# Kernel tuning notes

Measured on AMD Instinct MI355X. Metric: run time of the kernel, lower is better.

The kernel has to match this reference:

```python
import jax, jax.numpy as jnp
import numpy as np

IN_DIM = 1024
HID = 2048
BATCH = 8192


def setup_inputs() -> dict:
    key = jax.random.key(0)
    ks = jax.random.split(key, 10)
    s1 = 1.0 / np.sqrt(IN_DIM)
    s2 = 1.0 / np.sqrt(HID)
    inp = {
        "x": jax.random.normal(ks[0], (BATCH, IN_DIM), dtype=jnp.float32),
        "W1": jax.random.uniform(ks[1], (IN_DIM, HID), jnp.float32, -s1, s1),
        "b1": jax.random.uniform(ks[2], (HID,), jnp.float32, -s1, s1),
        "W2": jax.random.uniform(ks[3], (HID, HID), jnp.float32, -s2, s2),
        "b2": jax.random.uniform(ks[4], (HID,), jnp.float32, -s2, s2),
        "W3": jax.random.uniform(ks[5], (HID, HID), jnp.float32, -s2, s2),
        "b3": jax.random.uniform(ks[6], (HID,), jnp.float32, -s2, s2),
        "Wout": jax.random.uniform(ks[7], (HID, 1), jnp.float32, -s2, s2),
        "bout": jax.random.uniform(ks[8], (1,), jnp.float32, -s2, s2),
        "weight": jnp.array([0.1], dtype=jnp.float32),
        "bias": jnp.array([0.0], dtype=jnp.float32),
        "scale": jnp.array([1.0], dtype=jnp.float32),
        "shift": jnp.array([0.0], dtype=jnp.float32),
    }
    return inp


def reference(x, W1, b1, W2, b2, W3, b3, Wout, bout, weight, bias, scale, shift):
    # 3-layer tanh MLP core
    h = jnp.tanh(x @ W1 + b1)
    h = jnp.tanh(h @ W2 + b2)
    core_out = jnp.tanh(h @ W3 + b3)  # [B, HID]
    # Closed form of per-element 1-qubit statevector sim:
    # <Y> for RX(w) RY(v) H |0>  ==  sin(w) * sin(v)
    q_out = jnp.sin(weight[0]) * jnp.sin(core_out)
    q_out = (q_out + bias[0]) * scale[0] + shift[0]
    out = core_out + q_out
    out = out @ Wout + bout  # [B, 1]
    return out.squeeze(-1)  # [B]
```

## Files before the change

kernel.cpp:

```cpp
#include <hip/hip_runtime.h>
#include <hip/hip_bf16.h>


typedef _Float16 f16;
typedef __attribute__((ext_vector_type(8))) _Float16 f16x8;
typedef __attribute__((ext_vector_type(4))) _Float16 f16x4;
typedef __attribute__((ext_vector_type(4))) float f32x4;

#define BATCH 8192
#define IN_DIM 1024
#define HID 2048

__device__ __forceinline__ float fast_tanh(float x) {
  x = fminf(12.0f, fmaxf(-12.0f, x));
  float e = __expf(2.0f * x);
  return (e - 1.0f) * __builtin_amdgcn_rcpf(e + 1.0f);
}

__global__ __launch_bounds__(256) void cast_kernel(const float* __restrict__ in,
                                                   f16* __restrict__ out, int n4) {
  int i = blockIdx.x * blockDim.x + threadIdx.x;
  if (i < n4) {
    float4 v = reinterpret_cast<const float4*>(in)[i];
    f16x4 o = { (f16)v.x, (f16)v.y, (f16)v.z, (f16)v.w };
    reinterpret_cast<f16x4*>(out)[i] = o;
  }
}

__global__ __launch_bounds__(256) void transpose_cast_kernel(const float* __restrict__ W,
                                                             f16* __restrict__ Wt,
                                                             int K, int N) {
  __shared__ float tile[32][33];
  int kb = blockIdx.y * 32, nb = blockIdx.x * 32;
  int tx = threadIdx.x, ty = threadIdx.y;
#pragma unroll
  for (int i = 0; i < 4; ++i)
    tile[ty + i * 8][tx] = W[(size_t)(kb + ty + i * 8) * N + nb + tx];
  __syncthreads();
#pragma unroll
  for (int i = 0; i < 4; ++i)
    Wt[(size_t)(nb + ty + i * 8) * K + kb + tx] = (f16)tile[tx][ty + i * 8];
}


#define GLDS16(g, l)                                                         \
  __builtin_amdgcn_global_load_lds(                                          \
      (const __attribute__((address_space(1))) unsigned int*)(g),            \
      (__attribute__((address_space(3))) unsigned int*)(l), 16, 0, 0)

template <int K>
__global__ __launch_bounds__(512, 2) void gemm256_bias_tanh(
    const f16* __restrict__ A,
    const f16* __restrict__ Bt,
    const float* __restrict__ bias,
    f16* __restrict__ Out) {
  constexpr int NT = K / 32;
  __shared__ f16 As[4][8192];
  __shared__ f16 Bs[4][8192];

  const int T = threadIdx.x;
  const int l = T & 63;
  const int w = T >> 6;
  const int wm = w >> 2, wn = w & 3;
  const int lr = l & 15;
  const int lc = l >> 4;

  const int bm = (int)blockIdx.x >> 3;
  const int bn = (int)blockIdx.x & 7;
  const int tm = bm << 8, tn = bn << 8;

  const int srow = ((T >> 5) << 3) + (T & 7);
  const int skel = ((T >> 3) & 3) << 3;
  const f16* gA0 = A + (size_t)(tm + srow) * K + skel;
  const f16* gA1 = A + (size_t)(tm + srow + 128) * K + skel;
  const f16* gB0 = Bt + (size_t)(tn + srow) * K + skel;
  const f16* gB1 = Bt + (size_t)(tn + srow + 128) * K + skel;
  const int ldsw0 = w * 512;
  const int ldsw1 = 4096 + w * 512;

  const int abase = (wm * 16 + (lr >> 3)) * 256 + lc * 64 + (lr & 7) * 8;
  const int bbase = (wn * 8 + (lr >> 3)) * 256 + lc * 64 + (lr & 7) * 8;

  f32x4 acc[8][4] = {};

  GLDS16(gA0, &As[0][ldsw0]);
  GLDS16(gA1, &As[0][ldsw1]);
  GLDS16(gB0, &Bs[0][ldsw0]);
  GLDS16(gB1, &Bs[0][ldsw1]);
  GLDS16(gA0 + 32, &As[1][ldsw0]);
  GLDS16(gA1 + 32, &As[1][ldsw1]);
  GLDS16(gB0 + 32, &Bs[1][ldsw0]);
  GLDS16(gB1 + 32, &Bs[1][ldsw1]);
  asm volatile("s_waitcnt vmcnt(4)" ::: "memory");
  __builtin_amdgcn_s_barrier();
  __builtin_amdgcn_sched_barrier(0);

  for (int t = 0; t < NT; ++t) {
    const int q = t & 3;
    f16x8 afr[4], bfr[4];
#pragma unroll
    for (int mi = 0; mi < 4; ++mi)
      afr[mi] = *reinterpret_cast<const f16x8*>(&As[q][abase + mi * 512]);
#pragma unroll
    for (int ni = 0; ni < 4; ++ni)
      bfr[ni] = *reinterpret_cast<const f16x8*>(&Bs[q][bbase + ni * 512]);
    if (t + 2 < NT) {
      const int q2 = (t + 2) & 3;
      const int ko = (t + 2) * 32;
      GLDS16(gA0 + ko, &As[q2][ldsw0]);
      GLDS16(gA1 + ko, &As[q2][ldsw1]);
    }
    __builtin_amdgcn_s_barrier();
    asm volatile("s_waitcnt lgkmcnt(0)" ::: "memory");
    __builtin_amdgcn_sched_barrier(0);
    __builtin_amdgcn_s_setprio(1);
#pragma unroll
    for (int mi = 0; mi < 4; ++mi)
#pragma unroll
      for (int ni = 0; ni < 4; ++ni)
        acc[mi][ni] = __builtin_amdgcn_mfma_f32_16x16x32_f16(
            afr[mi], bfr[ni], acc[mi][ni], 0, 0, 0);
    __builtin_amdgcn_s_setprio(0);
    __builtin_amdgcn_s_barrier();
    __builtin_amdgcn_sched_barrier(0);

    f16x8 afr2[4];
#pragma unroll
    for (int mi = 0; mi < 4; ++mi)
      afr2[mi] = *reinterpret_cast<const f16x8*>(&As[q][abase + (4 + mi) * 512]);
    if (t + 2 < NT) {
      const int q2 = (t + 2) & 3;
      const int ko = (t + 2) * 32;
      GLDS16(gB0 + ko, &Bs[q2][ldsw0]);
      GLDS16(gB1 + ko, &Bs[q2][ldsw1]);
      asm volatile("s_waitcnt vmcnt(4)" ::: "memory");
    } else {
      asm volatile("s_waitcnt vmcnt(0)" ::: "memory");
    }
    __builtin_amdgcn_s_barrier();
    asm volatile("s_waitcnt lgkmcnt(0)" ::: "memory");
    __builtin_amdgcn_sched_barrier(0);
    __builtin_amdgcn_s_setprio(1);
#pragma unroll
    for (int mi = 0; mi < 4; ++mi)
#pragma unroll
      for (int ni = 0; ni < 4; ++ni)
        acc[4 + mi][ni] = __builtin_amdgcn_mfma_f32_16x16x32_f16(
            afr2[mi], bfr[ni], acc[4 + mi][ni], 0, 0, 0);
    __builtin_amdgcn_s_setprio(0);
    __builtin_amdgcn_s_barrier();
    __builtin_amdgcn_sched_barrier(0);
  }

#pragma unroll
  for (int ni = 0; ni < 4; ++ni) {
    const int col = tn + wn * 64 + ni * 16 + lr;
    const float bv = bias[col];
#pragma unroll
    for (int mi = 0; mi < 8; ++mi) {
      const int row0 = tm + wm * 128 + mi * 16 + ((l >> 4) << 2);
#pragma unroll
      for (int j = 0; j < 4; ++j) {
        float v = fast_tanh(acc[mi][ni][j] + bv);
        Out[(size_t)(row0 + j) * HID + col] = (f16)v;
      }
    }
  }
}

__global__ __launch_bounds__(256) void final_reduce(
    const f16* __restrict__ core, const float* __restrict__ Wout,
    const float* __restrict__ bout, const float* __restrict__ weight,
    const float* __restrict__ qbias, const float* __restrict__ qscale,
    const float* __restrict__ qshift, float* __restrict__ out) {
  const int b = blockIdx.x, t = threadIdx.x;
  const float sw = __sinf(weight[0]);
  const float qb = qbias[0], qs = qscale[0], qsh = qshift[0];
  f16x8 c8 = *reinterpret_cast<const f16x8*>(&core[(size_t)b * HID + t * 8]);
  float sum = 0.f;
#pragma unroll
  for (int j = 0; j < 8; ++j) {
    float c = (float)c8[j];
    float s = c + (sw * __sinf(c) + qb) * qs + qsh;
    sum += s * Wout[t * 8 + j];
  }
#pragma unroll
  for (int off = 32; off >= 1; off >>= 1) sum += __shfl_down(sum, off, 64);
  __shared__ float red[4];
  if ((t & 63) == 0) red[t >> 6] = sum;
  __syncthreads();
  if (t == 0) out[b] = red[0] + red[1] + red[2] + red[3] + bout[0];
}

extern "C" void kernel_launch(void* const* d_in, const int* in_sizes, int n_in,
                              void* d_out, int out_size, void* d_ws, size_t ws_size,
                              hipStream_t stream) {
  const float* x    = (const float*)d_in[0];
  const float* W1   = (const float*)d_in[1];
  const float* b1   = (const float*)d_in[2];
  const float* W2   = (const float*)d_in[3];
  const float* b2   = (const float*)d_in[4];
  const float* W3   = (const float*)d_in[5];
  const float* b3   = (const float*)d_in[6];
  const float* Wout = (const float*)d_in[7];
  const float* bout = (const float*)d_in[8];
  const float* wgt  = (const float*)d_in[9];
  const float* qb   = (const float*)d_in[10];
  const float* qs   = (const float*)d_in[11];
  const float* qsh  = (const float*)d_in[12];
  float* out = (float*)d_out;

  char* ws = (char*)d_ws;
  size_t off = 0;
  f16* xh  = (f16*)(ws + off); off += (size_t)BATCH * IN_DIM * sizeof(f16);
  f16* w1t = (f16*)(ws + off); off += (size_t)HID * IN_DIM * sizeof(f16);
  f16* w2t = (f16*)(ws + off); off += (size_t)HID * HID * sizeof(f16);
  f16* w3t = (f16*)(ws + off); off += (size_t)HID * HID * sizeof(f16);
  f16* h1  = (f16*)(ws + off); off += (size_t)BATCH * HID * sizeof(f16);
  f16* h2  = (f16*)(ws + off); off += (size_t)BATCH * HID * sizeof(f16);

  {
    int n4 = BATCH * IN_DIM / 4;
    cast_kernel<<<(n4 + 255) / 256, 256, 0, stream>>>(x, xh, n4);
  }
  {
    dim3 blk(32, 8);
    transpose_cast_kernel<<<dim3(HID / 32, IN_DIM / 32), blk, 0, stream>>>(W1, w1t, IN_DIM, HID);
    transpose_cast_kernel<<<dim3(HID / 32, HID / 32),    blk, 0, stream>>>(W2, w2t, HID, HID);
    transpose_cast_kernel<<<dim3(HID / 32, HID / 32),    blk, 0, stream>>>(W3, w3t, HID, HID);
  }
  const int grid = (BATCH / 256) * (HID / 256);
  gemm256_bias_tanh<IN_DIM><<<grid, 512, 0, stream>>>(xh, w1t, b1, h1);
  gemm256_bias_tanh<HID>   <<<grid, 512, 0, stream>>>(h1, w2t, b2, h2);
  gemm256_bias_tanh<HID>   <<<grid, 512, 0, stream>>>(h2, w3t, b3, h1);
  final_reduce<<<BATCH, 256, 0, stream>>>(h1, Wout, bout, wgt, qb, qs, qsh, out);
}
```

Measured before the change: 362.2 us.

## Deepen GEMM prefetch to three stages, merge weight transposes, stage epilogue through LDS

The GEMM main loop now prefetches three K-tiles ahead and loads both A and B tiles in one step. It replaces the two half-step phases with a single 8x4 MFMA block per iteration and one barrier, cutting synchronisation overhead. The epilogue writes tanh outputs into swizzled LDS and then stores 16-byte coalesced rows instead of scattered 2-byte stores. The three weight transpose launches are merged into one kernel. Holding all 8 A fragments at once raises register pressure, which may hurt occupancy at 2 blocks per CU.

```diff
diff --git a/kernel.cpp b/kernel.cpp
--- a/kernel.cpp
+++ b/kernel.cpp
@@ -27,12 +27,19 @@
   }
 }
 
-__global__ __launch_bounds__(256) void transpose_cast_kernel(const float* __restrict__ W,
-                                                             f16* __restrict__ Wt,
-                                                             int K, int N) {
+__global__ __launch_bounds__(256) void transpose_cast3(
+    const float* __restrict__ W1, const float* __restrict__ W2,
+    const float* __restrict__ W3, f16* __restrict__ w1t,
+    f16* __restrict__ w2t, f16* __restrict__ w3t) {
   __shared__ float tile[32][33];
-  int kb = blockIdx.y * 32, nb = blockIdx.x * 32;
-  int tx = threadIdx.x, ty = threadIdx.y;
+  int b = blockIdx.x;
+  const float* W; f16* Wt; int K, N;
+  if (b < 2048)      { W = W1; Wt = w1t; K = IN_DIM; N = HID; }
+  else if (b < 6144) { W = W2; Wt = w2t; K = HID;    N = HID; b -= 2048; }
+  else               { W = W3; Wt = w3t; K = HID;    N = HID; b -= 6144; }
+  const int nbt = N / 32;
+  const int nb = (b % nbt) * 32, kb = (b / nbt) * 32;
+  const int tx = threadIdx.x, ty = threadIdx.y;
 #pragma unroll
   for (int i = 0; i < 4; ++i)
     tile[ty + i * 8][tx] = W[(size_t)(kb + ty + i * 8) * N + nb + tx];
@@ -55,8 +62,9 @@
     const float* __restrict__ bias,
     f16* __restrict__ Out) {
   constexpr int NT = K / 32;
-  __shared__ f16 As[4][8192];
-  __shared__ f16 Bs[4][8192];
+  __shared__ f16 smem[65536];
+  f16* As = smem;
+  f16* Bs = smem + 32768;
 
   const int T = threadIdx.x;
   const int l = T & 63;
@@ -83,88 +91,86 @@
 
   f32x4 acc[8][4] = {};
 
-  GLDS16(gA0, &As[0][ldsw0]);
-  GLDS16(gA1, &As[0][ldsw1]);
-  GLDS16(gB0, &Bs[0][ldsw0]);
-  GLDS16(gB1, &Bs[0][ldsw1]);
-  GLDS16(gA0 + 32, &As[1][ldsw0]);
-  GLDS16(gA1 + 32, &As[1][ldsw1]);
-  GLDS16(gB0 + 32, &Bs[1][ldsw0]);
-  GLDS16(gB1 + 32, &Bs[1][ldsw1]);
-  asm volatile("s_waitcnt vmcnt(4)" ::: "memory");
+#pragma unroll
+  for (int p = 0; p < 3; ++p) {
+    const int ko = p * 32;
+    f16* aq = As + p * 8192;
+    f16* bq = Bs + p * 8192;
+    GLDS16(gA0 + ko, aq + ldsw0);
+    GLDS16(gA1 + ko, aq + ldsw1);
+    GLDS16(gB0 + ko, bq + ldsw0);
+    GLDS16(gB1 + ko, bq + ldsw1);
+  }
+  asm volatile("s_waitcnt vmcnt(8)" ::: "memory");
   __builtin_amdgcn_s_barrier();
   __builtin_amdgcn_sched_barrier(0);
 
   for (int t = 0; t < NT; ++t) {
     const int q = t & 3;
-    f16x8 afr[4], bfr[4];
-#pragma unroll
-    for (int mi = 0; mi < 4; ++mi)
-      afr[mi] = *reinterpret_cast<const f16x8*>(&As[q][abase + mi * 512]);
+    const f16* aq = As + q * 8192;
+    const f16* bq = Bs + q * 8192;
+    f16x8 afr[8], bfr[4];
+#pragma unroll
+    for (int mi = 0; mi < 8; ++mi)
+      afr[mi] = *reinterpret_cast<const f16x8*>(&aq[abase + mi * 512]);
 #pragma unroll
     for (int ni = 0; ni < 4; ++ni)
-      bfr[ni] = *reinterpret_cast<const f16x8*>(&Bs[q][bbase + ni * 512]);
-    if (t + 2 < NT) {
-      const int q2 = (t + 2) & 3;
-      const int ko = (t + 2) * 32;
-      GLDS16(gA0 + ko, &As[q2][ldsw0]);
-      GLDS16(gA1 + ko, &As[q2][ldsw1]);
+      bfr[ni] = *reinterpret_cast<const f16x8*>(&bq[bbase + ni * 512]);
+    if (t + 3 < NT) {
+      const int q3 = (t + 3) & 3;
+      const int ko = (t + 3) * 32;
+      f16* aw = As + q3 * 8192;
+      f16* bw = Bs + q3 * 8192;
+      GLDS16(gA0 + ko, aw + ldsw0);
+      GLDS16(gA1 + ko, aw + ldsw1);
+      GLDS16(gB0 + ko, bw + ldsw0);
+      GLDS16(gB1 + ko, bw + ldsw1);
     }
-    __builtin_amdgcn_s_barrier();
-    asm volatile("s_waitcnt lgkmcnt(0)" ::: "memory");
-    __builtin_amdgcn_sched_barrier(0);
     __builtin_amdgcn_s_setprio(1);
 #pragma unroll
-    for (int mi = 0; mi < 4; ++mi)
+    for (int mi = 0; mi < 8; ++mi)
 #pragma unroll
       for (int ni = 0; ni < 4; ++ni)
         acc[mi][ni] = __builtin_amdgcn_mfma_f32_16x16x32_f16(
             afr[mi], bfr[ni], acc[mi][ni], 0, 0, 0);
     __builtin_amdgcn_s_setprio(0);
-    __builtin_amdgcn_s_barrier();
-    __builtin_amdgcn_sched_barrier(0);
-
-    f16x8 afr2[4];
-#pragma unroll
-    for (int mi = 0; mi < 4; ++mi)
-      afr2[mi] = *reinterpret_cast<const f16x8*>(&As[q][abase + (4 + mi) * 512]);
-    if (t + 2 < NT) {
-      const int q2 = (t + 2) & 3;
-      const int ko = (t + 2) * 32;
-      GLDS16(gB0 + ko, &Bs[q2][ldsw0]);
-      GLDS16(gB1 + ko, &Bs[q2][ldsw1]);
+    if (t + 3 < NT) {
+      asm volatile("s_waitcnt vmcnt(8)" ::: "memory");
+    } else if (t + 2 < NT) {
       asm volatile("s_waitcnt vmcnt(4)" ::: "memory");
     } else {
       asm volatile("s_waitcnt vmcnt(0)" ::: "memory");
     }
     __builtin_amdgcn_s_barrier();
-    asm volatile("s_waitcnt lgkmcnt(0)" ::: "memory");
     __builtin_amdgcn_sched_barrier(0);
-    __builtin_amdgcn_s_setprio(1);
-#pragma unroll
-    for (int mi = 0; mi < 4; ++mi)
-#pragma unroll
-      for (int ni = 0; ni < 4; ++ni)
-        acc[4 + mi][ni] = __builtin_amdgcn_mfma_f32_16x16x32_f16(
-            afr2[mi], bfr[ni], acc[4 + mi][ni], 0, 0, 0);
-    __builtin_amdgcn_s_setprio(0);
-    __builtin_amdgcn_s_barrier();
-    __builtin_amdgcn_sched_barrier(0);
   }
 
 #pragma unroll
   for (int ni = 0; ni < 4; ++ni) {
-    const int col = tn + wn * 64 + ni * 16 + lr;
-    const float bv = bias[col];
+    const int col = wn * 64 + ni * 16 + lr;
+    const float bv = bias[tn + col];
 #pragma unroll
     for (int mi = 0; mi < 8; ++mi) {
-      const int row0 = tm + wm * 128 + mi * 16 + ((l >> 4) << 2);
+      const int r0 = wm * 128 + mi * 16 + ((l >> 4) << 2);
 #pragma unroll
       for (int j = 0; j < 4; ++j) {
-        float v = fast_tanh(acc[mi][ni][j] + bv);
-        Out[(size_t)(row0 + j) * HID + col] = (f16)v;
+        const int r = r0 + j;
+        const int bo = r * 512 + ((col * 2) ^ ((r & 7) << 4));
+        *reinterpret_cast<f16*>(reinterpret_cast<char*>(smem) + bo) =
+            (f16)fast_tanh(acc[mi][ni][j] + bv);
       }
     }
+  }
+  __syncthreads();
+#pragma unroll
+  for (int it = 0; it < 16; ++it) {
+    const int r = w * 32 + it * 2 + (l >> 5);
+    const int cb = (l & 31) * 16;
+    const int so = r * 512 + (cb ^ ((r & 7) << 4));
+    f16x8 v = *reinterpret_cast<const f16x8*>(
+        reinterpret_cast<const char*>(smem) + so);
+    *reinterpret_cast<f16x8*>(
+        reinterpret_cast<char*>(Out + (size_t)(tm + r) * HID + tn) + cb) = v;
   }
 }
 
@@ -225,9 +231,7 @@
   }
   {
     dim3 blk(32, 8);
-    transpose_cast_kernel<<<dim3(HID / 32, IN_DIM / 32), blk, 0, stream>>>(W1, w1t, IN_DIM, HID);
-    transpose_cast_kernel<<<dim3(HID / 32, HID / 32),    blk, 0, stream>>>(W2, w2t, HID, HID);
-    transpose_cast_kernel<<<dim3(HID / 32, HID / 32),    blk, 0, stream>>>(W3, w3t, HID, HID);
+    transpose_cast3<<<10240, blk, 0, stream>>>(W1, W2, W3, w1t, w2t, w3t);
   }
   const int grid = (BATCH / 256) * (HID / 256);
   gemm256_bias_tanh<IN_DIM><<<grid, 512, 0, stream>>>(xh, w1t, b1, h1);
```

After: 332.6 us. 1.09x faster.
